# Kernel optimization log

Hardware: AMD Instinct MI355X
Metric: run time of the kernel (lower is better)

Reference implementation:

```python
import jax, jax.numpy as jnp
import numpy as np

N, C, T, VQ, VK = 8, 64, 256, 90, 50
S, L = 4, 4  # num_subset, lag_len
EPS = 1e-5


def conv1x1(x, W, b):
    # x: [n, c_in, t, v], W: [c_out, c_in], b: [c_out]
    return jnp.einsum('oc,nctv->notv', W, x) + b[None, :, None, None]


def batchnorm(x, gamma, beta):
    # training-mode BatchNorm2d with batch statistics (biased variance)
    m = jnp.mean(x, axis=(0, 2, 3), keepdims=True)
    v = jnp.mean((x - m) ** 2, axis=(0, 2, 3), keepdims=True)
    xn = (x - m) * jax.lax.rsqrt(v + EPS)
    return xn * gamma[None, :, None, None] + beta[None, :, None, None]


def setup_inputs() -> dict:
    key = jax.random.key(0)
    ks = jax.random.split(key, 20)
    f = lambda k, shp: jax.random.normal(k, shp, dtype=jnp.float32)
    w = 0.05
    return {
        'x_q': f(ks[0], (N, C, T, VQ)),
        'x_k': f(ks[1], (N, C, T, VK)),
        'x_v': f(ks[2], (N, C, T, VK)),
        'Wq': f(ks[3], (S * C, C)) * w, 'bq': f(ks[4], (S * C,)) * w,
        'Wk': f(ks[5], (S * C, C)) * w, 'bk': f(ks[6], (S * C,)) * w,
        'Wv': f(ks[7], (C, C)) * w, 'bv': f(ks[8], (C,)) * w,
        'Wout': f(ks[9], (C, S * C)) * w, 'bout': f(ks[10], (C,)) * w,
        'gamma_out': jnp.ones((C,), jnp.float32), 'beta_out': jnp.zeros((C,), jnp.float32),
        'Wdown': f(ks[11], (C, C)) * w, 'bdown': f(ks[12], (C,)) * w,
        'gamma_down': jnp.ones((C,), jnp.float32), 'beta_down': jnp.zeros((C,), jnp.float32),
    }


def reference(x_q, x_k, x_v, Wq, bq, Wk, bk, Wv, bv, Wout, bout,
              gamma_out, beta_out, Wdown, bdown, gamma_down, beta_down):
    Tq = T - L
    # query projection on truncated window -> [n, s, c, Tq, VQ]
    q = conv1x1(x_q[:, :, :Tq, :], Wq, bq).reshape(N, S, C, Tq, VQ)
    # 1x1 conv commutes with time slicing: project keys once over full T
    k_full = conv1x1(x_k, Wk, bk).reshape(N, S, C, T, VK)
    scale = (C * Tq) ** 0.5
    # multi-lag scores, each [n, s, VQ, VK]
    atts = [jnp.einsum('nsctu,nsctv->nsuv', q, k_full[:, :, :, l:Tq + l, :]) / scale
            for l in range(L + 1)]
    stack = jnp.stack(atts)  # [L+1, n, s, VQ, VK]
    p_att = (jnp.max(stack, axis=0) + jnp.mean(stack, axis=0)) * 0.5
    att = jax.nn.softmax(p_att, axis=-1)  # dropout = identity (eval)
    v = conv1x1(x_v, Wv, bv)  # [n, c, T, VK]
    y = jnp.einsum('nsvu,nctu->nsctv', att, v)  # [n, s, c, T, VQ]
    y = y.reshape(N, S * C, T, VQ)
    y = batchnorm(conv1x1(y, Wout, bout), gamma_out, beta_out)
    d = batchnorm(conv1x1(x_q, Wdown, bdown), gamma_down, beta_down)
    return jax.nn.leaky_relu(d + y, 0.1)
```

## Files before the change

### kernel.cpp

```cpp
#include <hip/hip_runtime.h>
#include <hip/hip_bf16.h>

typedef __hip_bfloat16 bf16;
typedef __attribute__((ext_vector_type(8))) short short8;
typedef __attribute__((ext_vector_type(16))) float f32x16;

__device__ __forceinline__ float b2f(bf16 x) { return __bfloat162float(x); }
__device__ __forceinline__ bf16  f2b(float x) { return __float2bfloat16(x); }
__device__ __forceinline__ short f2bs(float x) {
    bf16 h = __float2bfloat16(x);
    return *reinterpret_cast<short*>(&h);
}
__device__ __forceinline__ float s2f(short s) {
    bf16 h; *reinterpret_cast<short*>(&h) = s; return __bfloat162float(h);
}
__device__ __forceinline__ void gload_lds16(const void* g, void* l) {
    __builtin_amdgcn_global_load_lds(
        (const __attribute__((address_space(1))) void*)g,
        (__attribute__((address_space(3))) void*)l, 16, 0, 0);
}

constexpr int N_ = 8, C_ = 64, T_ = 256, VQ_ = 90, VK_ = 50, S_ = 4, L_ = 4;
constexpr int Tq_ = T_ - L_;
constexpr int NL  = L_ + 1;
constexpr int COLS = T_ * VQ_;
constexpr float EPSf = 1e-5f;
constexpr int NSL = 16;

union SMemG {
    struct { short A[8 * 256 * 8]; short B[8 * 128 * 8]; } ab;
    short buf[4][64 * 66];
};

__global__ __launch_bounds__(64)
void k0_precompute(const float* __restrict__ Wq, const float* __restrict__ bq,
                   const float* __restrict__ Wk, const float* __restrict__ bk,
                   short* __restrict__ MtA, float* __restrict__ bMp,
                   float* __restrict__ wb, float* __restrict__ cb) {
    int s  = blockIdx.x >> 6;
    int ci = blockIdx.x & 63;
    int cj = threadIdx.x;
    float m = 0.f;
    for (int c = 0; c < C_; ++c)
        m += Wq[(s * C_ + c) * C_ + ci] * Wk[(s * C_ + c) * C_ + cj];
    MtA[((cj >> 3) * 256 + s * C_ + ci) * 8 + (cj & 7)] = f2bs(m);
    if (cj == 0) {
        float v = 0.f;
        for (int c = 0; c < C_; ++c)
            v += Wq[(s * C_ + c) * C_ + ci] * bk[s * C_ + c];
        bMp[s * C_ + ci] = v;
    }
    if (ci == 0) {
        float v = 0.f;
        for (int c = 0; c < C_; ++c)
            v += bq[s * C_ + c] * Wk[(s * C_ + c) * C_ + cj];
        wb[s * C_ + cj] = v;
        if (cj == 0) {
            float v2 = 0.f;
            for (int c = 0; c < C_; ++c)
                v2 += bq[s * C_ + c] * bk[s * C_ + c];
            cb[s] = v2;
        }
    }
}

__global__ __launch_bounds__(256)
void k0b_wos(const float* __restrict__ Wout, const float* __restrict__ bout,
             const float* __restrict__ Wv, const float* __restrict__ bv,
             short* __restrict__ WosA, float* __restrict__ bos) {
    int cj = blockIdx.x;
    __shared__ float wvcol[C_];
    if (threadIdx.x < C_) wvcol[threadIdx.x] = Wv[threadIdx.x * C_ + cj];
    __syncthreads();
    int p = threadIdx.x;
    int s = p >> 6, o = p & 63;
    float acc = 0.f;
    for (int c = 0; c < C_; ++c)
        acc += Wout[o * (S_ * C_) + s * C_ + c] * wvcol[c];
    WosA[((cj >> 3) * 256 + p) * 8 + (cj & 7)] = f2bs(acc);
    if (cj == 0 && p < C_) {
        float a = bout[p];
        for (int k = 0; k < S_ * C_; ++k)
            a += Wout[p * (S_ * C_) + k] * bv[k & 63];
        bos[p] = a;
    }
}

__global__ __launch_bounds__(256)
void k0c_xqt(const float* __restrict__ xq, short* __restrict__ xqT) {
    int tt = blockIdx.x;
    int g  = blockIdx.y;
    int n  = blockIdx.z;
    int t0 = tt * 4;
    __shared__ float lds[8 * 360];
    int tid = threadIdx.x;
    const float* src = xq + ((size_t)(n * 64 + g * 8) * 256 + t0) * 90;
#pragma unroll
    for (int i = tid; i < 720; i += 256) {
        int c = i / 90, r = i % 90;
        float4 v = *(const float4*)(src + (size_t)c * 23040 + r * 4);
        *(float4*)(&lds[c * 360 + r * 4]) = v;
    }
    __syncthreads();
    for (int e = tid; e < 4 * 96; e += 256) {
        int t = e / 96, u = e % 96;
        short8 pk;
#pragma unroll
        for (int j = 0; j < 8; ++j)
            pk[j] = (u < 90) ? f2bs(lds[j * 360 + t * 90 + u]) : (short)0;
        *(short8*)(xqT + (((size_t)(n * 8 + g) * 256 + t0 + t) * 96 + u) * 8) = pk;
    }
}

__global__ __launch_bounds__(256)
void k1_mfma(const float* __restrict__ x_k, const short* __restrict__ MtA,
             const float* __restrict__ bMp, short* __restrict__ kqT) {
    int tb = blockIdx.x, n = blockIdx.y;
    int t0 = tb * 2;
    __shared__ SMemG u;
    __shared__ float bmp_s[256];
    int tid = threadIdx.x;
    if (tid < 256) bmp_s[tid] = bMp[tid];
    for (int i = tid; i < 2048; i += 256)
        ((short8*)u.ab.A)[i] = ((const short8*)MtA)[i];
    for (int m = tid; m < 8 * 128; m += 256) {
        int kg = m >> 7, c = m & 127;
        int t = c >> 6, v = c & 63;
        short8 pk;
        if (v < VK_) {
            const float* src = x_k + ((size_t)(n * 64 + kg * 8) * 256 + t0 + t) * VK_ + v;
#pragma unroll
            for (int j = 0; j < 8; ++j) pk[j] = f2bs(src[(size_t)j * 256 * VK_]);
        } else {
#pragma unroll
            for (int j = 0; j < 8; ++j) pk[j] = 0;
        }
        *(short8*)(u.ab.B + m * 8) = pk;
    }
    __syncthreads();
    int wave = tid >> 6, lane = tid & 63, q = lane >> 5, c32 = lane & 31;
    f32x16 acc[2][4];
#pragma unroll
    for (int mt = 0; mt < 2; ++mt) {
#pragma unroll
        for (int r = 0; r < 16; ++r) {
            float b = bmp_s[wave * 64 + mt * 32 + (r & 3) + 8 * (r >> 2) + 4 * q];
#pragma unroll
            for (int nt = 0; nt < 4; ++nt) acc[mt][nt][r] = b;
        }
    }
#pragma unroll
    for (int ks = 0; ks < 4; ++ks) {
        int kg = 2 * ks + q;
        short8 a0 = *(const short8*)(u.ab.A + (kg * 256 + wave * 64 + c32) * 8);
        short8 a1 = *(const short8*)(u.ab.A + (kg * 256 + wave * 64 + 32 + c32) * 8);
#pragma unroll
        for (int nt = 0; nt < 4; ++nt) {
            short8 b = *(const short8*)(u.ab.B + (kg * 128 + nt * 32 + c32) * 8);
            acc[0][nt] = __builtin_amdgcn_mfma_f32_32x32x16_bf16(a0, b, acc[0][nt], 0, 0, 0);
            acc[1][nt] = __builtin_amdgcn_mfma_f32_32x32x16_bf16(a1, b, acc[1][nt], 0, 0, 0);
        }
    }
    __syncthreads();
    int ns = n * 4 + wave;
    for (int t = 0; t < 2; ++t) {
#pragma unroll
        for (int mt = 0; mt < 2; ++mt)
#pragma unroll
            for (int ntl = 0; ntl < 2; ++ntl) {
                f32x16 A = acc[mt][t * 2 + ntl];
                int cloc = ntl * 32 + c32;
#pragma unroll
                for (int r = 0; r < 16; ++r) {
                    int ci = mt * 32 + (r & 3) + 8 * (r >> 2) + 4 * q;
                    u.buf[wave][cloc * 66 + ci] = f2bs(A[r]);
                }
            }
        __syncthreads();
        if (lane < VK_) {
#pragma unroll
            for (int g = 0; g < 8; ++g) {
                short8 pk;
#pragma unroll
                for (int j = 0; j < 8; ++j) pk[j] = u.buf[wave][lane * 66 + g * 8 + j];
                *(short8*)(kqT + ((((size_t)ns * 8 + g) * 256 + t0 + t) * VK_ + lane) * 8) = pk;
            }
        }
        __syncthreads();
    }
}

__global__ __launch_bounds__(128)
void k3b_kbsum(const float* __restrict__ x_k, const float* __restrict__ wb,
               const float* __restrict__ cb, float* __restrict__ kbsum) {
    int cjg = blockIdx.x;
    int n = blockIdx.y;
    __shared__ float S[2][NL][VK_];
    for (int pr = threadIdx.x; pr < 2 * VK_; pr += 128) {
        int cjl = pr / VK_, v = pr % VK_;
        const float* base = x_k + ((size_t)(n * 64 + cjg * 2 + cjl) * 256) * VK_ + v;
        float a = 0.f;
        for (int t = 0; t < Tq_; ++t) a += base[t * VK_];
        S[cjl][0][v] = a;
        float run = a;
        for (int l = 1; l < NL; ++l) {
            run += base[(251 + l) * VK_] - base[(l - 1) * VK_];
            S[cjl][l][v] = run;
        }
    }
    __syncthreads();
    for (int e = threadIdx.x; e < S_ * NL * VK_; e += 128) {
        int s = e / (NL * VK_), r = e % (NL * VK_), l = r / VK_, v = r % VK_;
        float a = wb[s * 64 + cjg * 2] * S[0][l][v] + wb[s * 64 + cjg * 2 + 1] * S[1][l][v];
        if (cjg == 0) a += (float)Tq_ * cb[s];
        atomicAdd(&kbsum[((size_t)(n * 4 + s) * NL + l) * VK_ + v], a);
    }
}

__global__ __launch_bounds__(256)
void k3_mfma(const short* __restrict__ xqT, const short* __restrict__ kqT,
             float* __restrict__ partial) {
    int gx = blockIdx.x;
    int g = gx >> 1, half = gx & 1;
    int ns = blockIdx.y;
    int n = ns >> 2;
    __shared__ __align__(16) short sbuf[2][15872];
    int tid = threadIdx.x;
    int wave = tid >> 6, lane = tid & 63;
    int q = lane >> 5, nl = lane & 31;
    int n1 = wave * 64 + nl, n2 = n1 + 32;
    int nc1 = min(n1, 249), nc2 = min(n2, 249);
    int l1 = nc1 / VK_, v1 = nc1 % VK_;
    int l2 = nc2 / VK_, v2 = nc2 % VK_;
    int bo1 = ((q + l1) * VK_ + v1) * 8;
    int bo2 = ((q + l2) * VK_ + v2) * 8;
    int ao = (q * 96 + nl) * 8;
    f32x16 acc[6];
#pragma unroll
    for (int i = 0; i < 6; ++i)
#pragma unroll
        for (int r = 0; r < 16; ++r) acc[i][r] = 0.f;
    const short* asrc = xqT + (size_t)(n * 8 + g) * 256 * 768;
    const short* bsrc = kqT + (size_t)(ns * 8 + g) * 256 * 400;
    int c0 = half * 10, nch = half ? 11 : 10;
    int ncall = (wave == 3) ? 7 : 8;

    auto stage = [&](int buf, int ch) {
        int t0 = ch * 12;
        const short8* aS = (const short8*)(asrc + t0 * 768);
        const short8* bS = (const short8*)(bsrc + t0 * 400);
        char* db = (char*)(&sbuf[buf][0]);
        for (int it = 0; it < ncall; ++it) {
            int call = wave * 8 + it;
            int i = call * 64 + lane;
            const void* gsrc = (i < 1152) ? (const void*)(aS + i)
                                          : (const void*)(bS + min(i - 1152, 799));
            gload_lds16(gsrc, db + call * 1024);
        }
    };

    stage(0, c0);
    for (int ci = 0; ci < nch; ++ci) {
        int cur = ci & 1;
        if (ci + 1 < nch) {
            stage(cur ^ 1, c0 + ci + 1);
            if (wave == 3) asm volatile("s_waitcnt vmcnt(7)" ::: "memory");
            else           asm volatile("s_waitcnt vmcnt(8)" ::: "memory");
        } else {
            asm volatile("s_waitcnt vmcnt(0)" ::: "memory");
        }
        __builtin_amdgcn_s_barrier();
        const short* xa  = &sbuf[cur][0];
        const short* kbs = &sbuf[cur][9216];
#pragma unroll
        for (int ts = 0; ts < 6; ++ts) {
            short8 a0 = *(const short8*)(xa + ao + ts * 1536);
            short8 a1 = *(const short8*)(xa + ao + 256 + ts * 1536);
            short8 a2 = *(const short8*)(xa + ao + 512 + ts * 1536);
            short8 b0 = *(const short8*)(kbs + bo1 + ts * 800);
            short8 b1 = *(const short8*)(kbs + bo2 + ts * 800);
            acc[0] = __builtin_amdgcn_mfma_f32_32x32x16_bf16(a0, b0, acc[0], 0, 0, 0);
            acc[1] = __builtin_amdgcn_mfma_f32_32x32x16_bf16(a1, b0, acc[1], 0, 0, 0);
            acc[2] = __builtin_amdgcn_mfma_f32_32x32x16_bf16(a2, b0, acc[2], 0, 0, 0);
            acc[3] = __builtin_amdgcn_mfma_f32_32x32x16_bf16(a0, b1, acc[3], 0, 0, 0);
            acc[4] = __builtin_amdgcn_mfma_f32_32x32x16_bf16(a1, b1, acc[4], 0, 0, 0);
            acc[5] = __builtin_amdgcn_mfma_f32_32x32x16_bf16(a2, b1, acc[5], 0, 0, 0);
        }
        __builtin_amdgcn_s_barrier();
    }
#pragma unroll
    for (int inb = 0; inb < 2; ++inb) {
        int ng = wave * 64 + inb * 32 + nl;
        if (ng < 250) {
            int l = ng / VK_, v = ng % VK_;
            float* pb = partial + ((((size_t)ns * 5 + l) * 90) * NSL + gx) * VK_ + v;
#pragma unroll
            for (int iu = 0; iu < 3; ++iu) {
#pragma unroll
                for (int r = 0; r < 16; ++r) {
                    int u2 = iu * 32 + (r & 3) + 8 * (r >> 2) + 4 * q;
                    if (u2 < 90) pb[(size_t)u2 * NSL * VK_] = acc[inb * 3 + iu][r];
                }
            }
        }
    }
}

__global__ __launch_bounds__(256)
void k4_softmax(const float* __restrict__ partial, const float* __restrict__ kbsum,
                bf16* __restrict__ att) {
    int ug = blockIdx.x;
    int ns = blockIdx.y;
    int u0 = ug * 15;
    __shared__ float sred[NL * 15 * VK_];
    for (int idx = threadIdx.x; idx < NL * 15 * VK_; idx += 256) {
        int l = idx / (15 * VK_), r = idx % (15 * VK_);
        int u2 = r / VK_, v = r % VK_;
        const float* p = partial + (((size_t)(ns * NL + l) * 90 + u0 + u2) * NSL) * VK_ + v;
        float a = 0.f;
#pragma unroll
        for (int sl = 0; sl < NSL; ++sl) a += p[sl * VK_];
        sred[idx] = a;
    }
    __syncthreads();
    if (threadIdx.x < 15) {
        int u2 = threadIdx.x;
        const float inv_scale = rsqrtf((float)(C_ * Tq_));
        float pv[VK_];
        float pmax = -1e30f;
#pragma unroll
        for (int v = 0; v < VK_; ++v) {
            float mx = -1e30f, mn = 0.f;
#pragma unroll
            for (int l = 0; l < NL; ++l) {
                float sl = (sred[(l * 15 + u2) * VK_ + v] + kbsum[((size_t)ns * NL + l) * VK_ + v]) * inv_scale;
                mx = fmaxf(mx, sl); mn += sl;
            }
            pv[v] = 0.5f * (mx + mn * (1.f / NL));
            pmax = fmaxf(pmax, pv[v]);
        }
        float sum = 0.f;
#pragma unroll
        for (int v = 0; v < VK_; ++v) { pv[v] = __expf(pv[v] - pmax); sum += pv[v]; }
        float inv = 1.f / sum;
#pragma unroll
        for (int v = 0; v < VK_; ++v)
            att[((size_t)ns * VQ_ + u0 + u2) * VK_ + v] = f2b(pv[v] * inv);
    }
}

__global__ __launch_bounds__(256)
void k5_mfma(const float* __restrict__ x_v, const short* __restrict__ WosA,
             short* __restrict__ wv_pack) {
    int tb = blockIdx.x, n = blockIdx.y;
    int t0 = tb * 2;
    __shared__ SMemG u;
    int tid = threadIdx.x;
    for (int i = tid; i < 2048; i += 256)
        ((short8*)u.ab.A)[i] = ((const short8*)WosA)[i];
    for (int m = tid; m < 8 * 128; m += 256) {
        int kg = m >> 7, c = m & 127;
        int t = c >> 6, v = c & 63;
        short8 pk;
        if (v < VK_) {
            const float* src = x_v + ((size_t)(n * 64 + kg * 8) * 256 + t0 + t) * VK_ + v;
#pragma unroll
            for (int j = 0; j < 8; ++j) pk[j] = f2bs(src[(size_t)j * 256 * VK_]);
        } else {
#pragma unroll
            for (int j = 0; j < 8; ++j) pk[j] = 0;
        }
        *(short8*)(u.ab.B + m * 8) = pk;
    }
    __syncthreads();
    int wave = tid >> 6, lane = tid & 63, q = lane >> 5, c32 = lane & 31;
    f32x16 acc[2][4];
#pragma unroll
    for (int mt = 0; mt < 2; ++mt)
#pragma unroll
        for (int nt = 0; nt < 4; ++nt)
#pragma unroll
            for (int r = 0; r < 16; ++r) acc[mt][nt][r] = 0.f;
#pragma unroll
    for (int ks = 0; ks < 4; ++ks) {
        int kg = 2 * ks + q;
        short8 a0 = *(const short8*)(u.ab.A + (kg * 256 + wave * 64 + c32) * 8);
        short8 a1 = *(const short8*)(u.ab.A + (kg * 256 + wave * 64 + 32 + c32) * 8);
#pragma unroll
        for (int nt = 0; nt < 4; ++nt) {
            short8 b = *(const short8*)(u.ab.B + (kg * 128 + nt * 32 + c32) * 8);
            acc[0][nt] = __builtin_amdgcn_mfma_f32_32x32x16_bf16(a0, b, acc[0][nt], 0, 0, 0);
            acc[1][nt] = __builtin_amdgcn_mfma_f32_32x32x16_bf16(a1, b, acc[1][nt], 0, 0, 0);
        }
    }
    __syncthreads();
    for (int t = 0; t < 2; ++t) {
#pragma unroll
        for (int mt = 0; mt < 2; ++mt)
#pragma unroll
            for (int ntl = 0; ntl < 2; ++ntl) {
                f32x16 A = acc[mt][t * 2 + ntl];
                int cloc = ntl * 32 + c32;
#pragma unroll
                for (int r = 0; r < 16; ++r) {
                    int o = mt * 32 + (r & 3) + 8 * (r >> 2) + 4 * q;
                    u.buf[wave][cloc * 66 + o] = f2bs(A[r]);
                }
            }
        __syncthreads();
        short* dst = wv_pack + (((size_t)(n * 256 + t0 + t)) * 32 + wave * 8) * 512;
#pragma unroll
        for (int vg = 0; vg < 8; ++vg) {
            short8 pk;
#pragma unroll
            for (int j = 0; j < 8; ++j) pk[j] = u.buf[wave][(vg * 8 + j) * 66 + lane];
            *(short8*)(dst + (size_t)vg * 512 + lane * 8) = pk;
        }
        __syncthreads();
    }
}

__global__ __launch_bounds__(256)
void k6_mfma(const bf16* __restrict__ att, const short* __restrict__ wv_pack,
             const float* __restrict__ bos, bf16* __restrict__ out_pre) {
    int tc = blockIdx.x, n = blockIdx.y;
    __shared__ __align__(16) short att_p[32 * 96 * 8];
    __shared__ float bos_s[64];
    int tid = threadIdx.x;
    if (tid < 64) bos_s[tid] = bos[tid];
    for (int m = tid; m < 96 * 256; m += 256) {
        int u2 = m >> 8, k = m & 255;
        int s = k >> 6, vs = k & 63;
        short val = 0;
        if (u2 < 90 && vs < VK_) {
            bf16 h = att[((size_t)(n * 4 + s) * 90 + u2) * VK_ + vs];
            val = *reinterpret_cast<short*>(&h);
        }
        att_p[((k >> 3) * 96 + u2) * 8 + (k & 7)] = val;
    }
    __syncthreads();
    int wave = tid >> 6, lane = tid & 63;
    int q = lane >> 5, c = lane & 31;
    int t = tc * 4 + wave;
    f32x16 acc[6];
#pragma unroll
    for (int ot = 0; ot < 2; ++ot)
#pragma unroll
        for (int r = 0; r < 16; ++r) {
            float b = bos_s[ot * 32 + (r & 3) + 8 * (r >> 2) + 4 * q];
            acc[ot * 3 + 0][r] = b; acc[ot * 3 + 1][r] = b; acc[ot * 3 + 2][r] = b;
        }
    const short* wbase = wv_pack + (size_t)(n * 256 + t) * (32 * 512);
#pragma unroll
    for (int st = 0; st < 16; ++st) {
        int gq = 2 * st + q;
        short8 a0 = *(const short8*)(wbase + (gq * 64 + c) * 8);
        short8 a1 = *(const short8*)(wbase + (gq * 64 + 32 + c) * 8);
        short8 b0 = *(const short8*)(att_p + (gq * 96 + c) * 8);
        short8 b1 = *(const short8*)(att_p + (gq * 96 + 32 + c) * 8);
        short8 b2 = *(const short8*)(att_p + (gq * 96 + 64 + c) * 8);
        acc[0] = __builtin_amdgcn_mfma_f32_32x32x16_bf16(a0, b0, acc[0], 0, 0, 0);
        acc[1] = __builtin_amdgcn_mfma_f32_32x32x16_bf16(a0, b1, acc[1], 0, 0, 0);
        acc[2] = __builtin_amdgcn_mfma_f32_32x32x16_bf16(a0, b2, acc[2], 0, 0, 0);
        acc[3] = __builtin_amdgcn_mfma_f32_32x32x16_bf16(a1, b0, acc[3], 0, 0, 0);
        acc[4] = __builtin_amdgcn_mfma_f32_32x32x16_bf16(a1, b1, acc[4], 0, 0, 0);
        acc[5] = __builtin_amdgcn_mfma_f32_32x32x16_bf16(a1, b2, acc[5], 0, 0, 0);
    }
#pragma unroll
    for (int ot = 0; ot < 2; ++ot)
#pragma unroll
        for (int ut = 0; ut < 3; ++ut) {
            int u2 = ut * 32 + c;
            if (u2 < 90) {
                f32x16 A = acc[ot * 3 + ut];
#pragma unroll
                for (int r = 0; r < 16; ++r) {
                    int o = ot * 32 + (r & 3) + 8 * (r >> 2) + 4 * q;
                    out_pre[((size_t)(n * 64 + o) * 256 + t) * 90 + u2] = f2b(A[r]);
                }
            }
        }
}

__global__ __launch_bounds__(256)
void k7_mfma(const float* __restrict__ X, const float* __restrict__ W,
             const float* __restrict__ bias, bf16* __restrict__ out) {
    int cb = blockIdx.x, n = blockIdx.y;
    int col0 = cb * 256;
    __shared__ __align__(16) short A[8 * 64 * 8];
    __shared__ __align__(16) short B[8 * 256 * 8];
    __shared__ float bias_s[64];
    int tid = threadIdx.x;
    if (tid < 64) bias_s[tid] = bias[tid];
    for (int idx = tid; idx < 4096; idx += 256) {
        int o = idx >> 6, k = idx & 63;
        A[((k >> 3) * 64 + o) * 8 + (k & 7)] = f2bs(W[o * 64 + k]);
    }
    for (int m = tid; m < 8 * 256; m += 256) {
        int kg = m >> 8, c = m & 255;
        const float* src = X + (size_t)(n * 64 + kg * 8) * COLS + col0 + c;
        short8 pk;
#pragma unroll
        for (int j = 0; j < 8; ++j) pk[j] = f2bs(src[(size_t)j * COLS]);
        *(short8*)(B + m * 8) = pk;
    }
    __syncthreads();
    int wave = tid >> 6, lane = tid & 63, q = lane >> 5, c32 = lane & 31;
    f32x16 acc[2][2];
#pragma unroll
    for (int mt = 0; mt < 2; ++mt)
#pragma unroll
        for (int r = 0; r < 16; ++r) {
            float b = bias_s[mt * 32 + (r & 3) + 8 * (r >> 2) + 4 * q];
            acc[mt][0][r] = b; acc[mt][1][r] = b;
        }
#pragma unroll
    for (int ks = 0; ks < 4; ++ks) {
        int kg = 2 * ks + q;
        short8 a0 = *(const short8*)(A + (kg * 64 + c32) * 8);
        short8 a1 = *(const short8*)(A + (kg * 64 + 32 + c32) * 8);
#pragma unroll
        for (int i = 0; i < 2; ++i) {
            short8 b = *(const short8*)(B + (kg * 256 + (wave * 2 + i) * 32 + c32) * 8);
            acc[0][i] = __builtin_amdgcn_mfma_f32_32x32x16_bf16(a0, b, acc[0][i], 0, 0, 0);
            acc[1][i] = __builtin_amdgcn_mfma_f32_32x32x16_bf16(a1, b, acc[1][i], 0, 0, 0);
        }
    }
#pragma unroll
    for (int mt = 0; mt < 2; ++mt)
#pragma unroll
        for (int i = 0; i < 2; ++i) {
            int col = col0 + (wave * 2 + i) * 32 + c32;
#pragma unroll
            for (int r = 0; r < 16; ++r) {
                int o = mt * 32 + (r & 3) + 8 * (r >> 2) + 4 * q;
                out[(size_t)(n * 64 + o) * COLS + col] = f2b(acc[mt][i][r]);
            }
        }
}

__global__ __launch_bounds__(256)
void k8_stats(const bf16* __restrict__ out_pre, const bf16* __restrict__ d_pre,
              float* __restrict__ stats) {
    int path = blockIdx.x >> 9;
    int b = blockIdx.x & 511;
    int o = b >> 3, n = b & 7;
    const bf16* p = (path ? d_pre : out_pre) + ((size_t)n * C_ + o) * COLS;
    float s = 0.f, sq = 0.f;
    for (int i8 = threadIdx.x; i8 < COLS / 8; i8 += 256) {
        short8 v8 = *(const short8*)(p + i8 * 8);
#pragma unroll
        for (int j = 0; j < 8; ++j) {
            float x = s2f(v8[j]);
            s += x; sq += x * x;
        }
    }
#pragma unroll
    for (int off = 32; off > 0; off >>= 1) {
        s  += __shfl_down(s, off, 64);
        sq += __shfl_down(sq, off, 64);
    }
    __shared__ float red[8];
    int wid = threadIdx.x >> 6, lane = threadIdx.x & 63;
    if (lane == 0) { red[wid * 2] = s; red[wid * 2 + 1] = sq; }
    __syncthreads();
    if (threadIdx.x == 0) {
        float S = 0.f, Q = 0.f;
        for (int w2 = 0; w2 < 4; ++w2) { S += red[w2 * 2]; Q += red[w2 * 2 + 1]; }
        atomicAdd(&stats[path * 128 + o * 2], S);
        atomicAdd(&stats[path * 128 + o * 2 + 1], Q);
    }
}

__global__ __launch_bounds__(256)
void k9_final(const bf16* __restrict__ out_pre, const bf16* __restrict__ d_pre,
              const float* __restrict__ stats,
              const float* __restrict__ gamma_out, const float* __restrict__ beta_out,
              const float* __restrict__ gamma_down, const float* __restrict__ beta_down,
              float* __restrict__ out) {
    const float invM = 1.f / ((float)N_ * COLS);
    size_t total8 = (size_t)N_ * C_ * COLS / 8;
    size_t stride = (size_t)gridDim.x * blockDim.x;
    for (size_t i8 = (size_t)blockIdx.x * blockDim.x + threadIdx.x; i8 < total8; i8 += stride) {
        size_t idx = i8 * 8;
        int o = (int)((idx / COLS) % C_);
        float my = stats[o * 2] * invM;
        float vy = stats[o * 2 + 1] * invM - my * my;
        float md = stats[128 + o * 2] * invM;
        float vd = stats[128 + o * 2 + 1] * invM - md * md;
        float ay = rsqrtf(vy + EPSf) * gamma_out[o];
        float by = beta_out[o] - my * ay;
        float ad = rsqrtf(vd + EPSf) * gamma_down[o];
        float bd = beta_down[o] - md * ad;
        short8 y8 = *(const short8*)(out_pre + idx);
        short8 d8 = *(const short8*)(d_pre + idx);
        float rr[8];
#pragma unroll
        for (int j = 0; j < 8; ++j) {
            float r = (s2f(y8[j]) * ay + by) + (s2f(d8[j]) * ad + bd);
            rr[j] = r > 0.f ? r : 0.1f * r;
        }
        *(float4*)(out + idx)     = make_float4(rr[0], rr[1], rr[2], rr[3]);
        *(float4*)(out + idx + 4) = make_float4(rr[4], rr[5], rr[6], rr[7]);
    }
}

extern "C" void kernel_launch(void* const* d_in, const int* in_sizes, int n_in,
                              void* d_out, int out_size, void* d_ws, size_t ws_size,
                              hipStream_t stream) {
    (void)in_sizes; (void)n_in; (void)out_size; (void)ws_size;
    const float* x_q  = (const float*)d_in[0];
    const float* x_k  = (const float*)d_in[1];
    const float* x_v  = (const float*)d_in[2];
    const float* Wq   = (const float*)d_in[3];
    const float* bq   = (const float*)d_in[4];
    const float* Wk   = (const float*)d_in[5];
    const float* bk   = (const float*)d_in[6];
    const float* Wv   = (const float*)d_in[7];
    const float* bv   = (const float*)d_in[8];
    const float* Wout = (const float*)d_in[9];
    const float* bout = (const float*)d_in[10];
    const float* gamma_out  = (const float*)d_in[11];
    const float* beta_out   = (const float*)d_in[12];
    const float* Wdown = (const float*)d_in[13];
    const float* bdown = (const float*)d_in[14];
    const float* gamma_down = (const float*)d_in[15];
    const float* beta_down  = (const float*)d_in[16];

    char* w = (char*)d_ws;
    size_t off = 0;
    auto nxt = [&](size_t bytes) {
        char* p = w + off;
        off += (bytes + 255) & ~(size_t)255;
        return p;
    };
    short* MtA   = (short*)nxt((size_t)8 * 256 * 8 * 2);
    float* bMp   = (float*)nxt(256 * 4);
    float* wbp   = (float*)nxt((size_t)S_ * C_ * 4);
    float* cbp   = (float*)nxt((size_t)S_ * 4);
    short* WosA  = (short*)nxt((size_t)8 * 256 * 8 * 2);
    float* bos   = (float*)nxt((size_t)C_ * 4);
    float* kbsum = (float*)nxt((size_t)N_ * S_ * NL * VK_ * 4);
    bf16*  att   = (bf16*)nxt((size_t)N_ * S_ * VQ_ * VK_ * 2);
    float* stats = (float*)nxt(256 * 4);
    char* regionA = nxt((size_t)N_ * 8 * T_ * 96 * 8 * 2);
    short* xqT    = (short*)regionA;
    bf16*  out_pre = (bf16*)regionA;
    char* regionB = nxt((size_t)N_ * S_ * 8 * T_ * VK_ * 8 * 2);
    short* kqT   = (short*)regionB;
    bf16*  d_pre = (bf16*)regionB;
    char* regionC = nxt((size_t)N_ * T_ * 32 * 512 * 2);
    float* partial = (float*)regionC;
    short* wv_pack = (short*)regionC;

    hipMemsetAsync(stats, 0, 256 * 4, stream);
    hipMemsetAsync(kbsum, 0, (size_t)N_ * S_ * NL * VK_ * 4, stream);

    k0_precompute<<<S_ * C_, 64, 0, stream>>>(Wq, bq, Wk, bk, MtA, bMp, wbp, cbp);
    k0b_wos<<<C_, 256, 0, stream>>>(Wout, bout, Wv, bv, WosA, bos);
    k0c_xqt<<<dim3(64, 8, N_), 256, 0, stream>>>(x_q, xqT);
    k1_mfma<<<dim3(128, N_), 256, 0, stream>>>(x_k, MtA, bMp, kqT);
    k3b_kbsum<<<dim3(32, N_), 128, 0, stream>>>(x_k, wbp, cbp, kbsum);
    k3_mfma<<<dim3(NSL, N_ * S_), 256, 0, stream>>>(xqT, kqT, partial);
    k4_softmax<<<dim3(6, N_ * S_), 256, 0, stream>>>(partial, kbsum, att);
    k5_mfma<<<dim3(128, N_), 256, 0, stream>>>(x_v, WosA, wv_pack);
    k6_mfma<<<dim3(T_ / 4, N_), 256, 0, stream>>>(att, wv_pack, bos, out_pre);
    k7_mfma<<<dim3(COLS / 256, N_), 256, 0, stream>>>(x_q, Wdown, bdown, d_pre);
    k8_stats<<<1024, 256, 0, stream>>>(out_pre, d_pre, stats);
    k9_final<<<2880, 256, 0, stream>>>(out_pre, d_pre, stats, gamma_out, beta_out,
                                       gamma_down, beta_down, (float*)d_out);
}
```

Baseline: 392.2 us.

## Deepen k3 LDS pipeline to four stages and vectorize input staging via LDS

In k3, the double-buffered 12-timestep chunks become a four-buffer ring of 6-timestep chunks. The A tile is packed to 90 columns instead of 96, and vmcnt waits are tuned per wave to keep three loads in flight. This is meant to hide global latency better and cut LDS footprint. In k1, k5 and k7, the strided scalar fp32 gathers are replaced by coalesced float4 loads into an LDS scratch buffer, then transposed and packed to bf16. That adds barriers and LDS use but should improve memory coalescing.

Measured after the change: 402.2 us. +2.6%, slower.

```diff
diff --git a/kernel.cpp b/kernel.cpp
--- a/kernel.cpp
+++ b/kernel.cpp
@@ -119,25 +119,33 @@
     int t0 = tb * 2;
     __shared__ SMemG u;
     __shared__ float bmp_s[256];
+    __shared__ float xs[3200];
     int tid = threadIdx.x;
     if (tid < 256) bmp_s[tid] = bMp[tid];
     for (int i = tid; i < 2048; i += 256)
         ((short8*)u.ab.A)[i] = ((const short8*)MtA)[i];
-    for (int m = tid; m < 8 * 128; m += 256) {
-        int kg = m >> 7, c = m & 127;
-        int t = c >> 6, v = c & 63;
-        short8 pk;
-        if (v < VK_) {
-            const float* src = x_k + ((size_t)(n * 64 + kg * 8) * 256 + t0 + t) * VK_ + v;
-#pragma unroll
-            for (int j = 0; j < 8; ++j) pk[j] = f2bs(src[(size_t)j * 256 * VK_]);
-        } else {
-#pragma unroll
-            for (int j = 0; j < 8; ++j) pk[j] = 0;
-        }
-        *(short8*)(u.ab.B + m * 8) = pk;
-    }
-    __syncthreads();
+#pragma unroll
+    for (int p = 0; p < 2; ++p) {
+        for (int i4 = tid; i4 < 800; i4 += 256) {
+            int c32 = i4 / 25, o = i4 % 25;
+            *(float4*)(&xs[c32 * 100 + o * 4]) =
+                *(const float4*)(x_k + ((size_t)(n * 64 + p * 32 + c32) * 256 + t0) * 50 + o * 4);
+        }
+        __syncthreads();
+        for (int m = tid; m < 512; m += 256) {
+            int kgl = m >> 7, c = m & 127, t = c >> 6, v = c & 63;
+            short8 pk;
+            if (v < VK_) {
+#pragma unroll
+                for (int j = 0; j < 8; ++j) pk[j] = f2bs(xs[(kgl * 8 + j) * 100 + t * 50 + v]);
+            } else {
+#pragma unroll
+                for (int j = 0; j < 8; ++j) pk[j] = 0;
+            }
+            *(short8*)(u.ab.B + ((p * 4 + kgl) * 128 + c) * 8) = pk;
+        }
+        __syncthreads();
+    }
     int wave = tid >> 6, lane = tid & 63, q = lane >> 5, c32 = lane & 31;
     f32x16 acc[2][4];
 #pragma unroll
@@ -224,7 +232,7 @@
     int g = gx >> 1, half = gx & 1;
     int ns = blockIdx.y;
     int n = ns >> 2;
-    __shared__ __align__(16) short sbuf[2][15872];
+    __shared__ __align__(16) short sbuf[4][8704];
     int tid = threadIdx.x;
     int wave = tid >> 6, lane = tid & 63;
     int q = lane >> 5, nl = lane & 31;
@@ -234,49 +242,58 @@
     int l2 = nc2 / VK_, v2 = nc2 % VK_;
     int bo1 = ((q + l1) * VK_ + v1) * 8;
     int bo2 = ((q + l2) * VK_ + v2) * 8;
-    int ao = (q * 96 + nl) * 8;
+    int ao = (q * 90 + nl) * 8;
     f32x16 acc[6];
 #pragma unroll
     for (int i = 0; i < 6; ++i)
 #pragma unroll
         for (int r = 0; r < 16; ++r) acc[i][r] = 0.f;
-    const short* asrc = xqT + (size_t)(n * 8 + g) * 256 * 768;
-    const short* bsrc = kqT + (size_t)(ns * 8 + g) * 256 * 400;
-    int c0 = half * 10, nch = half ? 11 : 10;
-    int ncall = (wave == 3) ? 7 : 8;
+    const short8* asrc8 = (const short8*)(xqT + (size_t)(n * 8 + g) * 256 * 768);
+    const short8* bsrc8 = (const short8*)(kqT + (size_t)(ns * 8 + g) * 256 * 400);
+    int c0 = half * 21;
+    int myst = (wave == 0) ? 0 : 1 + wave * 4;
+    int mync = (wave == 0) ? 5 : 4;
 
     auto stage = [&](int buf, int ch) {
-        int t0 = ch * 12;
-        const short8* aS = (const short8*)(asrc + t0 * 768);
-        const short8* bS = (const short8*)(bsrc + t0 * 400);
+        int t0 = ch * 6;
         char* db = (char*)(&sbuf[buf][0]);
-        for (int it = 0; it < ncall; ++it) {
-            int call = wave * 8 + it;
-            int i = call * 64 + lane;
-            const void* gsrc = (i < 1152) ? (const void*)(aS + i)
-                                          : (const void*)(bS + min(i - 1152, 799));
-            gload_lds16(gsrc, db + call * 1024);
+        for (int it = 0; it < mync; ++it) {
+            int k = myst + it;
+            int i = k * 64 + lane;
+            const void* gsrc;
+            if (i < 540) {
+                int t = i / 90, uu = i - t * 90;
+                gsrc = (const void*)(asrc8 + (t0 + t) * 96 + uu);
+            } else {
+                int b = i - 540; if (b > 499) b = 499;
+                gsrc = (const void*)(bsrc8 + t0 * 50 + b);
+            }
+            gload_lds16(gsrc, db + k * 1024);
         }
     };
 
-    stage(0, c0);
-    for (int ci = 0; ci < nch; ++ci) {
-        int cur = ci & 1;
-        if (ci + 1 < nch) {
-            stage(cur ^ 1, c0 + ci + 1);
-            if (wave == 3) asm volatile("s_waitcnt vmcnt(7)" ::: "memory");
-            else           asm volatile("s_waitcnt vmcnt(8)" ::: "memory");
-        } else {
-            asm volatile("s_waitcnt vmcnt(0)" ::: "memory");
+    stage(0, c0); stage(1, c0 + 1); stage(2, c0 + 2);
+    for (int ci = 0; ci < 21; ++ci) {
+        if (ci < 18) stage((ci + 3) & 3, c0 + ci + 3);
+        int rem = 20 - ci; if (rem > 3) rem = 3;
+        int w = rem * mync;
+        switch (w) {
+            case 15: asm volatile("s_waitcnt vmcnt(15)" ::: "memory"); break;
+            case 12: asm volatile("s_waitcnt vmcnt(12)" ::: "memory"); break;
+            case 10: asm volatile("s_waitcnt vmcnt(10)" ::: "memory"); break;
+            case 8:  asm volatile("s_waitcnt vmcnt(8)"  ::: "memory"); break;
+            case 5:  asm volatile("s_waitcnt vmcnt(5)"  ::: "memory"); break;
+            case 4:  asm volatile("s_waitcnt vmcnt(4)"  ::: "memory"); break;
+            default: asm volatile("s_waitcnt vmcnt(0)"  ::: "memory"); break;
         }
         __builtin_amdgcn_s_barrier();
-        const short* xa  = &sbuf[cur][0];
-        const short* kbs = &sbuf[cur][9216];
-#pragma unroll
-        for (int ts = 0; ts < 6; ++ts) {
-            short8 a0 = *(const short8*)(xa + ao + ts * 1536);
-            short8 a1 = *(const short8*)(xa + ao + 256 + ts * 1536);
-            short8 a2 = *(const short8*)(xa + ao + 512 + ts * 1536);
+        const short* xa  = &sbuf[ci & 3][0];
+        const short* kbs = &sbuf[ci & 3][4320];
+#pragma unroll
+        for (int ts = 0; ts < 3; ++ts) {
+            short8 a0 = *(const short8*)(xa + ao + ts * 1440);
+            short8 a1 = *(const short8*)(xa + ao + 256 + ts * 1440);
+            short8 a2 = *(const short8*)(xa + ao + 512 + ts * 1440);
             short8 b0 = *(const short8*)(kbs + bo1 + ts * 800);
             short8 b1 = *(const short8*)(kbs + bo2 + ts * 800);
             acc[0] = __builtin_amdgcn_mfma_f32_32x32x16_bf16(a0, b0, acc[0], 0, 0, 0);
@@ -355,24 +372,32 @@
     int tb = blockIdx.x, n = blockIdx.y;
     int t0 = tb * 2;
     __shared__ SMemG u;
+    __shared__ float xs[3200];
     int tid = threadIdx.x;
     for (int i = tid; i < 2048; i += 256)
         ((short8*)u.ab.A)[i] = ((const short8*)WosA)[i];
-    for (int m = tid; m < 8 * 128; m += 256) {
-        int kg = m >> 7, c = m & 127;
-        int t = c >> 6, v = c & 63;
-        short8 pk;
-        if (v < VK_) {
-            const float* src = x_v + ((size_t)(n * 64 + kg * 8) * 256 + t0 + t) * VK_ + v;
-#pragma unroll
-            for (int j = 0; j < 8; ++j) pk[j] = f2bs(src[(size_t)j * 256 * VK_]);
-        } else {
-#pragma unroll
-            for (int j = 0; j < 8; ++j) pk[j] = 0;
-        }
-        *(short8*)(u.ab.B + m * 8) = pk;
-    }
-    __syncthreads();
+#pragma unroll
+    for (int p = 0; p < 2; ++p) {
+        for (int i4 = tid; i4 < 800; i4 += 256) {
+            int c32 = i4 / 25, o = i4 % 25;
+            *(float4*)(&xs[c32 * 100 + o * 4]) =
+                *(const float4*)(x_v + ((size_t)(n * 64 + p * 32 + c32) * 256 + t0) * 50 + o * 4);
+        }
+        __syncthreads();
+        for (int m = tid; m < 512; m += 256) {
+            int kgl = m >> 7, c = m & 127, t = c >> 6, v = c & 63;
+            short8 pk;
+            if (v < VK_) {
+#pragma unroll
+                for (int j = 0; j < 8; ++j) pk[j] = f2bs(xs[(kgl * 8 + j) * 100 + t * 50 + v]);
+            } else {
+#pragma unroll
+                for (int j = 0; j < 8; ++j) pk[j] = 0;
+            }
+            *(short8*)(u.ab.B + ((p * 4 + kgl) * 128 + c) * 8) = pk;
+        }
+        __syncthreads();
+    }
     int wave = tid >> 6, lane = tid & 63, q = lane >> 5, c32 = lane & 31;
     f32x16 acc[2][4];
 #pragma unroll
@@ -490,21 +515,29 @@
     __shared__ __align__(16) short A[8 * 64 * 8];
     __shared__ __align__(16) short B[8 * 256 * 8];
     __shared__ float bias_s[64];
+    __shared__ float xs[2048];
     int tid = threadIdx.x;
     if (tid < 64) bias_s[tid] = bias[tid];
     for (int idx = tid; idx < 4096; idx += 256) {
         int o = idx >> 6, k = idx & 63;
         A[((k >> 3) * 64 + o) * 8 + (k & 7)] = f2bs(W[o * 64 + k]);
     }
-    for (int m = tid; m < 8 * 256; m += 256) {
-        int kg = m >> 8, c = m & 255;
-        const float* src = X + (size_t)(n * 64 + kg * 8) * COLS + col0 + c;
-        short8 pk;
-#pragma unroll
-        for (int j = 0; j < 8; ++j) pk[j] = f2bs(src[(size_t)j * COLS]);
-        *(short8*)(B + m * 8) = pk;
-    }
-    __syncthreads();
+#pragma unroll
+    for (int p = 0; p < 8; ++p) {
+        for (int i4 = tid; i4 < 512; i4 += 256) {
+            int cl = i4 >> 6, o = i4 & 63;
+            *(float4*)(&xs[cl * 256 + o * 4]) =
+                *(const float4*)(X + (size_t)(n * 64 + p * 8 + cl) * COLS + col0 + o * 4);
+        }
+        __syncthreads();
+        {
+            short8 pk;
+#pragma unroll
+            for (int j = 0; j < 8; ++j) pk[j] = f2bs(xs[j * 256 + tid]);
+            *(short8*)(B + (p * 256 + tid) * 8) = pk;
+        }
+        __syncthreads();
+    }
     int wave = tid >> 6, lane = tid & 63, q = lane >> 5, c32 = lane & 31;
     f32x16 acc[2][2];
 #pragma unroll
```

## Stage fp32 input tiles via float4 loads in LDS; remap k3 blocks; raise MFMA priority

Applied to the files above, without the earlier changes.

The k1, k5 and k7 projection kernels now load their fp32 input rows into a shared-memory staging buffer with coalesced float4 global loads. They then transpose and pack to bf16 from LDS, replacing scalar strided global reads. The k3 score kernel remaps its block index so blocks that share the same xqT slice are scheduled close together, for better L2 reuse. It also raises wave priority around the MFMA loop. The staging adds extra LDS usage and barriers, which may reduce occupancy.

After: 403.3 us. 1.03x slower.

```diff
diff --git a/kernel.cpp b/kernel.cpp
--- a/kernel.cpp
+++ b/kernel.cpp
@@ -119,25 +119,33 @@
     int t0 = tb * 2;
     __shared__ SMemG u;
     __shared__ float bmp_s[256];
+    __shared__ float xs[3200];
     int tid = threadIdx.x;
     if (tid < 256) bmp_s[tid] = bMp[tid];
     for (int i = tid; i < 2048; i += 256)
         ((short8*)u.ab.A)[i] = ((const short8*)MtA)[i];
-    for (int m = tid; m < 8 * 128; m += 256) {
-        int kg = m >> 7, c = m & 127;
-        int t = c >> 6, v = c & 63;
-        short8 pk;
-        if (v < VK_) {
-            const float* src = x_k + ((size_t)(n * 64 + kg * 8) * 256 + t0 + t) * VK_ + v;
-#pragma unroll
-            for (int j = 0; j < 8; ++j) pk[j] = f2bs(src[(size_t)j * 256 * VK_]);
-        } else {
-#pragma unroll
-            for (int j = 0; j < 8; ++j) pk[j] = 0;
-        }
-        *(short8*)(u.ab.B + m * 8) = pk;
-    }
-    __syncthreads();
+#pragma unroll
+    for (int p = 0; p < 2; ++p) {
+        for (int i4 = tid; i4 < 800; i4 += 256) {
+            int c32 = i4 / 25, o = i4 % 25;
+            *(float4*)(&xs[c32 * 100 + o * 4]) =
+                *(const float4*)(x_k + ((size_t)(n * 64 + p * 32 + c32) * 256 + t0) * 50 + o * 4);
+        }
+        __syncthreads();
+        for (int m = tid; m < 512; m += 256) {
+            int kgl = m >> 7, c = m & 127, t = c >> 6, v = c & 63;
+            short8 pk;
+            if (v < VK_) {
+#pragma unroll
+                for (int j = 0; j < 8; ++j) pk[j] = f2bs(xs[(kgl * 8 + j) * 100 + t * 50 + v]);
+            } else {
+#pragma unroll
+                for (int j = 0; j < 8; ++j) pk[j] = 0;
+            }
+            *(short8*)(u.ab.B + ((p * 4 + kgl) * 128 + c) * 8) = pk;
+        }
+        __syncthreads();
+    }
     int wave = tid >> 6, lane = tid & 63, q = lane >> 5, c32 = lane & 31;
     f32x16 acc[2][4];
 #pragma unroll
@@ -220,10 +228,15 @@
 __global__ __launch_bounds__(256)
 void k3_mfma(const short* __restrict__ xqT, const short* __restrict__ kqT,
              float* __restrict__ partial) {
-    int gx = blockIdx.x;
-    int g = gx >> 1, half = gx & 1;
-    int ns = blockIdx.y;
-    int n = ns >> 2;
+    int lin = blockIdx.x + 16 * blockIdx.y;
+    int grp = lin & 7;
+    int idx = lin >> 3;
+    int slice = grp + 8 * (idx >> 3);
+    int sub = idx & 7;
+    int n = slice >> 3, g = slice & 7;
+    int s = sub >> 1, half = sub & 1;
+    int ns = n * 4 + s;
+    int gx = g * 2 + half;
     __shared__ __align__(16) short sbuf[2][15872];
     int tid = threadIdx.x;
     int wave = tid >> 6, lane = tid & 63;
@@ -272,6 +285,7 @@
         __builtin_amdgcn_s_barrier();
         const short* xa  = &sbuf[cur][0];
         const short* kbs = &sbuf[cur][9216];
+        __builtin_amdgcn_s_setprio(1);
 #pragma unroll
         for (int ts = 0; ts < 6; ++ts) {
             short8 a0 = *(const short8*)(xa + ao + ts * 1536);
@@ -286,6 +300,7 @@
             acc[4] = __builtin_amdgcn_mfma_f32_32x32x16_bf16(a1, b1, acc[4], 0, 0, 0);
             acc[5] = __builtin_amdgcn_mfma_f32_32x32x16_bf16(a2, b1, acc[5], 0, 0, 0);
         }
+        __builtin_amdgcn_s_setprio(0);
         __builtin_amdgcn_s_barrier();
     }
 #pragma unroll
@@ -355,24 +370,32 @@
     int tb = blockIdx.x, n = blockIdx.y;
     int t0 = tb * 2;
     __shared__ SMemG u;
+    __shared__ float xs[3200];
     int tid = threadIdx.x;
     for (int i = tid; i < 2048; i += 256)
         ((short8*)u.ab.A)[i] = ((const short8*)WosA)[i];
-    for (int m = tid; m < 8 * 128; m += 256) {
-        int kg = m >> 7, c = m & 127;
-        int t = c >> 6, v = c & 63;
-        short8 pk;
-        if (v < VK_) {
-            const float* src = x_v + ((size_t)(n * 64 + kg * 8) * 256 + t0 + t) * VK_ + v;
-#pragma unroll
-            for (int j = 0; j < 8; ++j) pk[j] = f2bs(src[(size_t)j * 256 * VK_]);
-        } else {
-#pragma unroll
-            for (int j = 0; j < 8; ++j) pk[j] = 0;
-        }
-        *(short8*)(u.ab.B + m * 8) = pk;
-    }
-    __syncthreads();
+#pragma unroll
+    for (int p = 0; p < 2; ++p) {
+        for (int i4 = tid; i4 < 800; i4 += 256) {
+            int c32 = i4 / 25, o = i4 % 25;
+            *(float4*)(&xs[c32 * 100 + o * 4]) =
+                *(const float4*)(x_v + ((size_t)(n * 64 + p * 32 + c32) * 256 + t0) * 50 + o * 4);
+        }
+        __syncthreads();
+        for (int m = tid; m < 512; m += 256) {
+            int kgl = m >> 7, c = m & 127, t = c >> 6, v = c & 63;
+            short8 pk;
+            if (v < VK_) {
+#pragma unroll
+                for (int j = 0; j < 8; ++j) pk[j] = f2bs(xs[(kgl * 8 + j) * 100 + t * 50 + v]);
+            } else {
+#pragma unroll
+                for (int j = 0; j < 8; ++j) pk[j] = 0;
+            }
+            *(short8*)(u.ab.B + ((p * 4 + kgl) * 128 + c) * 8) = pk;
+        }
+        __syncthreads();
+    }
     int wave = tid >> 6, lane = tid & 63, q = lane >> 5, c32 = lane & 31;
     f32x16 acc[2][4];
 #pragma unroll
@@ -490,21 +513,29 @@
     __shared__ __align__(16) short A[8 * 64 * 8];
     __shared__ __align__(16) short B[8 * 256 * 8];
     __shared__ float bias_s[64];
+    __shared__ float xs[2048];
     int tid = threadIdx.x;
     if (tid < 64) bias_s[tid] = bias[tid];
     for (int idx = tid; idx < 4096; idx += 256) {
         int o = idx >> 6, k = idx & 63;
         A[((k >> 3) * 64 + o) * 8 + (k & 7)] = f2bs(W[o * 64 + k]);
     }
-    for (int m = tid; m < 8 * 256; m += 256) {
-        int kg = m >> 8, c = m & 255;
-        const float* src = X + (size_t)(n * 64 + kg * 8) * COLS + col0 + c;
-        short8 pk;
-#pragma unroll
-        for (int j = 0; j < 8; ++j) pk[j] = f2bs(src[(size_t)j * COLS]);
-        *(short8*)(B + m * 8) = pk;
-    }
-    __syncthreads();
+#pragma unroll
+    for (int p = 0; p < 8; ++p) {
+        for (int i4 = tid; i4 < 512; i4 += 256) {
+            int cl = i4 >> 6, o = i4 & 63;
+            *(float4*)(&xs[cl * 256 + o * 4]) =
+                *(const float4*)(X + (size_t)(n * 64 + p * 8 + cl) * COLS + col0 + o * 4);
+        }
+        __syncthreads();
+        {
+            short8 pk;
+#pragma unroll
+            for (int j = 0; j < 8; ++j) pk[j] = f2bs(xs[j * 256 + tid]);
+            *(short8*)(B + (p * 256 + tid) * 8) = pk;
+        }
+        __syncthreads();
+    }
     int wave = tid >> 6, lane = tid & 63, q = lane >> 5, c32 = lane & 31;
     f32x16 acc[2][2];
 #pragma unroll
```
